# Optimization experiments

Measured on AMD Instinct MI355X. Metric: run time of the kernel, lower is better.

## Reference

```python
import jax, jax.numpy as jnp
import numpy as np

B, T, E = 256, 33, 1024
L = T - 1  # one distinct LSTM per timestep


def setup_inputs() -> dict:
    key = jax.random.key(0)
    k1, k2, k3, k4 = jax.random.split(key, 4)
    scale = 1.0 / np.sqrt(E)  # matches nn.LSTM default uniform init
    return {
        "input_feature_vectors": jax.random.normal(k1, (B, T, E), jnp.float32),
        "target_feature_vector": jax.random.normal(k2, (B, E), jnp.float32),
        "W_ih": jax.random.uniform(k3, (L, 4 * E, E), jnp.float32, -scale, scale),
        "W_hh": jax.random.uniform(k4, (L, 4 * E, E), jnp.float32, -scale, scale),
    }


def _lstm_step(carry, inp):
    h, c = carry                      # [B, E] each
    x_t, w_ih, w_hh = inp             # [B, E], [4E, E], [4E, E]
    gates = x_t @ w_ih.T + h @ w_hh.T  # [B, 4E]; bias=False in the original
    i, f, g, o = jnp.split(gates, 4, axis=-1)  # torch gate order: i, f, g, o
    i = jax.nn.sigmoid(i)
    f = jax.nn.sigmoid(f)
    g = jnp.tanh(g)
    o = jax.nn.sigmoid(o)
    c = f * c + i * g
    h = o * jnp.tanh(c)
    return (h, c), None


def reference(input_feature_vectors, target_feature_vector, W_ih, W_hh):
    x = input_feature_vectors
    b, t, e = x.shape
    h0 = jnp.zeros((b, e), x.dtype)            # h_0 = zeros(1, B, E)
    c0 = x[:, 1, :]                            # c_0 = input[:, 1:2, :].transpose(0,1)
    xs = jnp.swapaxes(x[:, : t - 1, :], 0, 1)  # [T-1, B, E], steps 0..T-2
    (h, c), _ = jax.lax.scan(_lstm_step, (h0, c0), (xs, W_ih, W_hh))
    # output[:, 0, :] of the last step is the final h
    loss = jnp.mean(jnp.abs(h - target_feature_vector))  # L1Loss (mean)
    return loss, h, c
```

## Files before the change

kernel.cpp:

```cpp
#include <hip/hip_runtime.h>
#include <hip/hip_bf16.h>

typedef __attribute__((ext_vector_type(8))) short bf16x8;
typedef __attribute__((ext_vector_type(4))) float f32x4;
typedef __attribute__((ext_vector_type(16))) float f32x16;

static constexpr int BB = 256;
static constexpr int TT = 33;
static constexpr int EE = 1024;
static constexpr int LL = 32;
static constexpr int NG = 4096;

static constexpr int BUF_SZ   = 24576;
static constexpr int A_OFF    = 16384;
static constexpr int RED_OFF  = 98304;
static constexpr int LDSG_OFF = 131072;
static constexpr int HH_OFF   = 147456;
static constexpr int LDS_DYN  = 149504;

__device__ __forceinline__ short f2bf(float f) {
  unsigned u = __builtin_bit_cast(unsigned, f);
  u += 0x7fffu + ((u >> 16) & 1u);
  return (short)(u >> 16);
}

__device__ __forceinline__ bf16x8 cvt8(f32x4 a, f32x4 b) {
  bf16x8 r;
  r[0] = f2bf(a[0]); r[1] = f2bf(a[1]); r[2] = f2bf(a[2]); r[3] = f2bf(a[3]);
  r[4] = f2bf(b[0]); r[5] = f2bf(b[1]); r[6] = f2bf(b[2]); r[7] = f2bf(b[3]);
  return r;
}

__device__ __forceinline__ float sigm(float x) { return 1.0f / (1.0f + __expf(-x)); }
__device__ __forceinline__ float tanh_f(float x) { return 1.0f - 2.0f / (__expf(2.0f * x) + 1.0f); }

__global__ __launch_bounds__(256) void lstm_prep(
    const float* __restrict__ x, short* __restrict__ xbf, float* __restrict__ c_io,
    unsigned* __restrict__ flags)
{
  if (blockIdx.x == 0) flags[(size_t)threadIdx.x * 64] = 0;
  int gth = blockIdx.x * 256 + threadIdx.x;
  int eb  = gth & 127;
  int row = (gth >> 7) & 255;
  int t   = gth >> 15;
  const float* src = x + ((size_t)row * TT + t) * EE + (eb << 3);
  f32x4 lo = *(const f32x4*)src;
  f32x4 hi = *(const f32x4*)(src + 4);
  *(bf16x8*)(xbf + ((size_t)t * BB + row) * EE + (eb << 3)) = cvt8(lo, hi);
  if (t == 1) {
    float* cd = c_io + (size_t)row * EE + (eb << 3);
    *(f32x4*)cd = lo;
    *(f32x4*)(cd + 4) = hi;
  }
}

__global__ __launch_bounds__(512) void lstm_rec(
    const short* __restrict__ xbf,
    const float* __restrict__ Wih,
    const float* __restrict__ Whh,
    short* __restrict__ hroll,
    float* __restrict__ c_io,
    float* __restrict__ h_out,
    unsigned* __restrict__ flags)
{
  extern __shared__ __align__(16) char smem[];

  const int tid  = threadIdx.x;
  const int lane = tid & 63;
  const int wv   = tid >> 6;
  const int ct   = wv & 1;
  const int kh   = wv >> 1;

  const int wg     = blockIdx.x;
  const int xcd    = wg & 7;
  const int jj     = wg >> 3;
  const int rowgrp = jj & 3;
  const int ehi    = jj >> 2;
  const int e0     = (xcd * 8 + ehi) << 4;
  const int row0   = rowgrp << 6;

  size_t wsrc_off[2]; int wdst_off[2];
#pragma unroll
  for (int r = 0; r < 2; ++r) {
    int o = r * 8192 + wv * 1024 + lane * 16;
    int lrow = o >> 8;
    int mwr = ((lrow & 7) << 5) | ((lrow & 8) << 1);
    wsrc_off[r] = (size_t)((lrow >> 4) * EE + e0 + (lrow & 15)) * 4096 + ((o & 255) ^ mwr);
    wdst_off[r] = r * 8192 + wv * 1024;
  }
  size_t asrc_off; int adst_off;
  {
    int o = wv * 1024 + lane * 16;
    int lrow = o >> 7;
    asrc_off = (size_t)(row0 + lrow) * 2048 + ((o & 127) ^ ((lrow & 7) << 4));
    adst_off = A_OFF + wv * 1024;
  }

  const int wrow    = ct * 32 + (lane & 31);
  const int mwr2    = ((wrow & 7) << 5) | ((wrow & 8) << 1);
  const int kW      = kh * 64 + ((lane >> 5) << 5);
  const int woff_lo = wrow * 256 + (kW ^ mwr2);
  const int woff_hi = wrow * 256 + ((kW + 16) ^ mwr2);
  const int arow    = lane & 31;
  const int kA      = kh * 32 + ((lane >> 5) << 4);
  const int aoff0   = arow * 128 + (kA ^ ((arow & 7) << 4));
  const int aoff1   = aoff0 + 4096;

  const int er  = tid & 63;
  const int ee_ = tid >> 6;
  float c0r = c_io[(size_t)(row0 + er) * EE + e0 + ee_];
  float c1r = c_io[(size_t)(row0 + er) * EE + e0 + ee_ + 8];

  f32x16 acc0{}, acc1{};

  auto stageC = [&](int tt, int cc, int buf) {
    const int p  = cc >> 4;
    const int k0 = (cc & 15) << 6;
    const char* Wt = (const char*)((p ? Whh : Wih) + (size_t)tt * NG * EE);
    const char* At = p ? (const char*)(hroll + (size_t)(tt - 1) * BB * EE)
                       : (const char*)(xbf + (size_t)tt * BB * EE);
    char* dst = smem + buf * BUF_SZ;
#pragma unroll
    for (int r = 0; r < 2; ++r)
      __builtin_amdgcn_global_load_lds(
          (const __attribute__((address_space(1))) unsigned int*)(Wt + wsrc_off[r] + (k0 << 2)),
          (__attribute__((address_space(3))) unsigned int*)(dst + wdst_off[r]), 16, 0, 0);
    __builtin_amdgcn_global_load_lds(
        (const __attribute__((address_space(1))) unsigned int*)(At + asrc_off + (k0 << 1)),
        (__attribute__((address_space(3))) unsigned int*)(dst + adst_off), 16, 0, 0);
  };

  auto compute = [&](int buf) {
    const char* Wb = smem + buf * BUF_SZ;
    const char* Ab = Wb + A_OFF;
    f32x4 wlo = *(const f32x4*)(Wb + woff_lo);
    f32x4 whi = *(const f32x4*)(Wb + woff_hi);
    bf16x8 bfr = cvt8(wlo, whi);
    bf16x8 a0 = *(const bf16x8*)(Ab + aoff0);
    bf16x8 a1 = *(const bf16x8*)(Ab + aoff1);
    acc0 = __builtin_amdgcn_mfma_f32_32x32x16_bf16(a0, bfr, acc0, 0, 0, 0);
    acc1 = __builtin_amdgcn_mfma_f32_32x32x16_bf16(a1, bfr, acc1, 0, 0, 0);
  };

  float* red = (float*)(smem + RED_OFF);
  const int rsw = (lane & 3) << 4;
  auto slotp = [&](int src, int rt) { return red + (size_t)(((ct * 2 + src) * 2 + rt)) * 1024; };
  auto dumpT = [&](float* base, const f32x16& a) {
    char* b = (char*)base + lane * 64;
#pragma unroll
    for (int jq = 0; jq < 4; ++jq) {
      f32x4 v{a[jq * 4 + 0], a[jq * 4 + 1], a[jq * 4 + 2], a[jq * 4 + 3]};
      *(f32x4*)(b + ((jq * 16) ^ rsw)) = v;
    }
  };
  auto addT = [&](const float* base, f32x16& a) {
    const char* b = (const char*)base + lane * 64;
#pragma unroll
    for (int jq = 0; jq < 4; ++jq) {
      f32x4 v = *(const f32x4*)(b + ((jq * 16) ^ rsw));
      a[jq * 4 + 0] += v[0]; a[jq * 4 + 1] += v[1];
      a[jq * 4 + 2] += v[2]; a[jq * 4 + 3] += v[3];
    }
  };

  stageC(0, 0, 0);
  stageC(0, 1, 1);
  stageC(0, 2, 2);

  int fc = 0;
  for (int t = 0; t < LL; ++t) {
    const int nch = t ? 32 : 16;
    for (int c = 0; c < nch; ++c, ++fc) {
      if (t == LL - 1 && c == nch - 1)      asm volatile("s_waitcnt vmcnt(0)" ::: "memory");
      else if (t == LL - 1 && c == nch - 2) asm volatile("s_waitcnt vmcnt(3)" ::: "memory");
      else                                   asm volatile("s_waitcnt vmcnt(6)" ::: "memory");
      __builtin_amdgcn_s_barrier();
      compute(fc & 3);

      int sc = c + 3, st = t;
      if (sc >= nch) { sc -= nch; st = t + 1; }
      bool skip = (st > t && sc == 2) || (st >= LL);
      if (!skip) {
        if (st == t && sc == 16) {
          if (tid < 256) {
            while (__hip_atomic_load(flags + (size_t)tid * 64,
                                     __ATOMIC_RELAXED, __HIP_MEMORY_SCOPE_AGENT) < (unsigned)t)
              __builtin_amdgcn_s_sleep(1);
          }
          __builtin_amdgcn_s_barrier();
          __builtin_amdgcn_sched_barrier(0);
        }
        stageC(st, sc, (fc + 3) & 3);
      }
    }

    if (kh >= 2) { dumpT(slotp(kh - 2, 0), acc0); dumpT(slotp(kh - 2, 1), acc1); }
    asm volatile("s_waitcnt lgkmcnt(0)" ::: "memory");
    __builtin_amdgcn_s_barrier();
    if (kh < 2) { addT(slotp(kh, 0), acc0); addT(slotp(kh, 1), acc1); }
    asm volatile("s_waitcnt lgkmcnt(0)" ::: "memory");
    __builtin_amdgcn_s_barrier();
    if (kh == 1) { dumpT(slotp(0, 0), acc0); dumpT(slotp(0, 1), acc1); }
    asm volatile("s_waitcnt lgkmcnt(0)" ::: "memory");
    __builtin_amdgcn_s_barrier();
    if (kh == 0) {
      addT(slotp(0, 0), acc0);
      addT(slotp(0, 1), acc1);
      const int swc = mwr2;
      char* gb = (char*)(smem + LDSG_OFF) + wrow * 256;
#pragma unroll
      for (int rt = 0; rt < 2; ++rt) {
        const f32x16& a = rt ? acc1 : acc0;
#pragma unroll
        for (int jq = 0; jq < 4; ++jq) {
          int rowb = rt * 128 + jq * 32 + ((lane >> 5) << 4);
          f32x4 v{a[jq * 4 + 0], a[jq * 4 + 1], a[jq * 4 + 2], a[jq * 4 + 3]};
          *(f32x4*)(gb + (rowb ^ swc)) = v;
        }
      }
    }
    acc0 = f32x16{}; acc1 = f32x16{};
    asm volatile("s_waitcnt lgkmcnt(0)" ::: "memory");
    __builtin_amdgcn_s_barrier();

    {
      const char* gbase = (const char*)(smem + LDSG_OFF);
      short* hh = (short*)(smem + HH_OFF);
      auto gate = [&](int g, int ee) {
        int wc = g * 16 + ee;
        int swc = ((wc & 7) << 5) | ((wc & 8) << 1);
        return *(const float*)(gbase + wc * 256 + ((er * 4) ^ swc));
      };
      float gi0 = gate(0, ee_), gf0 = gate(1, ee_), gg0 = gate(2, ee_), go0 = gate(3, ee_);
      float gi1 = gate(0, ee_ + 8), gf1 = gate(1, ee_ + 8), gg1 = gate(2, ee_ + 8), go1 = gate(3, ee_ + 8);

      c0r = sigm(gf0) * c0r + sigm(gi0) * tanh_f(gg0);
      float h0n = sigm(go0) * tanh_f(c0r);
      c1r = sigm(gf1) * c1r + sigm(gi1) * tanh_f(gg1);
      float h1n = sigm(go1) * tanh_f(c1r);

      hh[er * 16 + ee_]     = f2bf(h0n);
      hh[er * 16 + ee_ + 8] = f2bf(h1n);

      if (t == LL - 1) {
        size_t o0 = (size_t)(row0 + er) * EE + e0 + ee_;
        size_t o1 = o0 + 8;
        h_out[o0] = h0n; c_io[o0] = c0r;
        h_out[o1] = h1n; c_io[o1] = c1r;
      }
    }
    asm volatile("s_waitcnt lgkmcnt(0)" ::: "memory");
    __builtin_amdgcn_s_barrier();

    if (t < LL - 1) {
      if (tid < 256) {
        int r = tid >> 2, q = tid & 3;
        unsigned long long v = *(const unsigned long long*)(smem + HH_OFF + r * 32 + q * 8);
        __hip_atomic_store(
            (unsigned long long*)((char*)hroll + ((size_t)t * BB + row0 + r) * 2048 + (size_t)e0 * 2 + q * 8),
            v, __ATOMIC_RELAXED, __HIP_MEMORY_SCOPE_AGENT);
      }
      stageC(t + 1, 2, (fc + 2) & 3);
      asm volatile("s_waitcnt vmcnt(3)" ::: "memory");
      __builtin_amdgcn_s_barrier();
      if (tid == 0)
        __hip_atomic_store(flags + (size_t)wg * 64, (unsigned)(t + 1),
                           __ATOMIC_RELAXED, __HIP_MEMORY_SCOPE_AGENT);
    }
  }
}

__global__ __launch_bounds__(256) void lstm_loss_part(
    const float* __restrict__ h, const float* __restrict__ tgt, float* __restrict__ partials)
{
  __shared__ float lds[4];
  int tid = threadIdx.x;
  float s = 0.f;
  int base = blockIdx.x * 1024 + tid;
#pragma unroll
  for (int q = 0; q < 4; ++q) {
    int idx = base + (q << 8);
    s += fabsf(h[idx] - tgt[idx]);
  }
#pragma unroll
  for (int off = 32; off > 0; off >>= 1) s += __shfl_down(s, off, 64);
  if ((tid & 63) == 0) lds[tid >> 6] = s;
  __syncthreads();
  if (tid == 0) partials[blockIdx.x] = lds[0] + lds[1] + lds[2] + lds[3];
}

__global__ __launch_bounds__(256) void lstm_loss_fin(
    const float* __restrict__ partials, float* __restrict__ out)
{
  __shared__ float lds[4];
  int tid = threadIdx.x;
  float s = partials[tid];
#pragma unroll
  for (int off = 32; off > 0; off >>= 1) s += __shfl_down(s, off, 64);
  if ((tid & 63) == 0) lds[tid >> 6] = s;
  __syncthreads();
  if (tid == 0) out[0] = (lds[0] + lds[1] + lds[2] + lds[3]) * (1.0f / 262144.0f);
}

extern "C" void kernel_launch(void* const* d_in, const int* in_sizes, int n_in,
                              void* d_out, int out_size, void* d_ws, size_t ws_size,
                              hipStream_t stream) {
  const float* x   = (const float*)d_in[0];
  const float* tgt = (const float*)d_in[1];
  const float* Wih = (const float*)d_in[2];
  const float* Whh = (const float*)d_in[3];

  float* out   = (float*)d_out;
  float* h_out = out + 1;
  float* c_io  = out + 1 + BB * EE;

  short* xbf      = (short*)d_ws;
  short* hroll    = (short*)((char*)xbf + (size_t)LL * BB * EE * 2);
  float* partials = (float*)((char*)hroll + (size_t)LL * BB * EE * 2);
  unsigned* flags = (unsigned*)((char*)partials + 1024);

  static bool attr_done = false;
  if (!attr_done) {
    hipFuncSetAttribute((const void*)lstm_rec,
                        hipFuncAttributeMaxDynamicSharedMemorySize, LDS_DYN);
    attr_done = true;
  }

  lstm_prep<<<4096, 256, 0, stream>>>(x, xbf, c_io, flags);

  {
    const short* xbfA = xbf; const float* WihA = Wih; const float* WhhA = Whh;
    short* hrollA = hroll; float* cA = c_io; float* hA = h_out; unsigned* flagsA = flags;
    void* args[] = {&xbfA, &WihA, &WhhA, &hrollA, &cA, &hA, &flagsA};
    hipError_t e = hipLaunchCooperativeKernel((void*)lstm_rec, dim3(256), dim3(512),
                                              args, LDS_DYN, stream);
    if (e != hipSuccess)
      lstm_rec<<<256, 512, LDS_DYN, stream>>>(xbf, Wih, Whh, hroll, c_io, h_out, flags);
  }

  lstm_loss_part<<<256, 256, 0, stream>>>(h_out, tgt, partials);
  lstm_loss_fin<<<1, 256, 0, stream>>>(partials, out);
}
```

Before: 609.4 us.

## Process K-chunks in pairs with six LDS buffers and reuse buffers for reduction

Each barrier now covers two K-chunks, with a six-deep LDS ring buffer replacing the four-deep one, so the main loop needs half as many barriers and waitcnt stalls. The cross-wave reduction scratch and the gate/h staging area now live in free ring buffers instead of dedicated LDS regions, which shrinks total LDS. The A-tile layout and swizzle are remapped so two rows share a 256-byte line, which changes the bank-conflict pattern. The cost is deeper in-flight prefetch, more complex buffer indexing, and a risk of buffer aliasing races at step boundaries.

```diff
diff --git a/kernel.cpp b/kernel.cpp
--- a/kernel.cpp
+++ b/kernel.cpp
@@ -11,12 +11,10 @@
 static constexpr int LL = 32;
 static constexpr int NG = 4096;
 
-static constexpr int BUF_SZ   = 24576;
-static constexpr int A_OFF    = 16384;
-static constexpr int RED_OFF  = 98304;
-static constexpr int LDSG_OFF = 131072;
-static constexpr int HH_OFF   = 147456;
-static constexpr int LDS_DYN  = 149504;
+static constexpr int BUF_SZ  = 24576;
+static constexpr int A_OFF   = 16384;
+static constexpr int NBUF    = 6;
+static constexpr int LDS_DYN = 147456;
 
 __device__ __forceinline__ short f2bf(float f) {
   unsigned u = __builtin_bit_cast(unsigned, f);
@@ -90,10 +88,14 @@
   }
   size_t asrc_off; int adst_off;
   {
-    int o = wv * 1024 + lane * 16;
-    int lrow = o >> 7;
-    asrc_off = (size_t)(row0 + lrow) * 2048 + ((o & 127) ^ ((lrow & 7) << 4));
-    adst_off = A_OFF + wv * 1024;
+    int o  = wv * 1024 + lane * 16;
+    int G  = o >> 4;
+    int rp = G >> 4;
+    int s  = G & 15;
+    int r  = rp * 2 + (s & 1);
+    int g  = ((s >> 1) ^ (rp & 7)) & 7;
+    asrc_off = (size_t)(row0 + r) * 2048 + g * 16;
+    adst_off = A_OFF + o;
   }
 
   const int wrow    = ct * 32 + (lane & 31);
@@ -102,9 +104,10 @@
   const int woff_lo = wrow * 256 + (kW ^ mwr2);
   const int woff_hi = wrow * 256 + ((kW + 16) ^ mwr2);
   const int arow    = lane & 31;
-  const int kA      = kh * 32 + ((lane >> 5) << 4);
-  const int aoff0   = arow * 128 + (kA ^ ((arow & 7) << 4));
-  const int aoff1   = aoff0 + 4096;
+  const int rpA     = arow >> 1;
+  const int gkh     = kh * 2 + (lane >> 5);
+  const int sA      = (2 * gkh + (arow & 1)) ^ ((rpA & 7) << 1);
+  const int aoff0   = rpA * 256 + sA * 16;
 
   const int er  = tid & 63;
   const int ee_ = tid >> 6;
@@ -137,14 +140,12 @@
     f32x4 whi = *(const f32x4*)(Wb + woff_hi);
     bf16x8 bfr = cvt8(wlo, whi);
     bf16x8 a0 = *(const bf16x8*)(Ab + aoff0);
-    bf16x8 a1 = *(const bf16x8*)(Ab + aoff1);
+    bf16x8 a1 = *(const bf16x8*)(Ab + aoff0 + 4096);
     acc0 = __builtin_amdgcn_mfma_f32_32x32x16_bf16(a0, bfr, acc0, 0, 0, 0);
     acc1 = __builtin_amdgcn_mfma_f32_32x32x16_bf16(a1, bfr, acc1, 0, 0, 0);
   };
 
-  float* red = (float*)(smem + RED_OFF);
-  const int rsw = (lane & 3) << 4;
-  auto slotp = [&](int src, int rt) { return red + (size_t)(((ct * 2 + src) * 2 + rt)) * 1024; };
+  const int rsw = ((lane >> 1) & 3) << 4;
   auto dumpT = [&](float* base, const f32x16& a) {
     char* b = (char*)base + lane * 64;
 #pragma unroll
@@ -163,25 +164,23 @@
     }
   };
 
-  stageC(0, 0, 0);
-  stageC(0, 1, 1);
-  stageC(0, 2, 2);
-
-  int fc = 0;
+  stageC(0, 0, 0); stageC(0, 1, 1); stageC(0, 2, 2); stageC(0, 3, 3);
+
+  int fb = 0;
   for (int t = 0; t < LL; ++t) {
     const int nch = t ? 32 : 16;
-    for (int c = 0; c < nch; ++c, ++fc) {
-      if (t == LL - 1 && c == nch - 1)      asm volatile("s_waitcnt vmcnt(0)" ::: "memory");
-      else if (t == LL - 1 && c == nch - 2) asm volatile("s_waitcnt vmcnt(3)" ::: "memory");
+    for (int pc = 0; pc < nch / 2; ++pc) {
+      if (t == LL - 1 && pc == nch / 2 - 1) asm volatile("s_waitcnt vmcnt(0)" ::: "memory");
       else                                   asm volatile("s_waitcnt vmcnt(6)" ::: "memory");
       __builtin_amdgcn_s_barrier();
-      compute(fc & 3);
-
-      int sc = c + 3, st = t;
-      if (sc >= nch) { sc -= nch; st = t + 1; }
-      bool skip = (st > t && sc == 2) || (st >= LL);
+      compute(fb);
+      compute((fb + 1) % NBUF);
+
+      int sc0 = 2 * pc + 4, st = t;
+      if (sc0 >= nch) { sc0 -= nch; st = t + 1; }
+      bool skip = (st > t && sc0 == 2) || (st >= LL);
       if (!skip) {
-        if (st == t && sc == 16) {
+        if (st == t && sc0 == 16) {
           if (tid < 256) {
             while (__hip_atomic_load(flags + (size_t)tid * 64,
                                      __ATOMIC_RELAXED, __HIP_MEMORY_SCOPE_AGENT) < (unsigned)t)
@@ -190,9 +189,15 @@
           __builtin_amdgcn_s_barrier();
           __builtin_amdgcn_sched_barrier(0);
         }
-        stageC(st, sc, (fc + 3) & 3);
+        stageC(st, sc0,     (fb + 4) % NBUF);
+        stageC(st, sc0 + 1, (fb + 5) % NBUF);
       }
-    }
+      fb = (fb + 2) % NBUF;
+    }
+
+    float* red  = (float*)(smem + (size_t)((fb + 4) % NBUF) * BUF_SZ);
+    char*  glsb = smem + (size_t)((fb + 5) % NBUF) * BUF_SZ;
+    auto slotp = [&](int src, int rt) { return red + (size_t)((ct * 2 + src) * 2 + rt) * 1024; };
 
     if (kh >= 2) { dumpT(slotp(kh - 2, 0), acc0); dumpT(slotp(kh - 2, 1), acc1); }
     asm volatile("s_waitcnt lgkmcnt(0)" ::: "memory");
@@ -206,8 +211,7 @@
     if (kh == 0) {
       addT(slotp(0, 0), acc0);
       addT(slotp(0, 1), acc1);
-      const int swc = mwr2;
-      char* gb = (char*)(smem + LDSG_OFF) + wrow * 256;
+      char* gb = glsb + wrow * 256;
 #pragma unroll
       for (int rt = 0; rt < 2; ++rt) {
         const f32x16& a = rt ? acc1 : acc0;
@@ -215,7 +219,7 @@
         for (int jq = 0; jq < 4; ++jq) {
           int rowb = rt * 128 + jq * 32 + ((lane >> 5) << 4);
           f32x4 v{a[jq * 4 + 0], a[jq * 4 + 1], a[jq * 4 + 2], a[jq * 4 + 3]};
-          *(f32x4*)(gb + (rowb ^ swc)) = v;
+          *(f32x4*)(gb + (rowb ^ mwr2)) = v;
         }
       }
     }
@@ -224,12 +228,11 @@
     __builtin_amdgcn_s_barrier();
 
     {
-      const char* gbase = (const char*)(smem + LDSG_OFF);
-      short* hh = (short*)(smem + HH_OFF);
+      short* hh = (short*)(glsb + 16384);
       auto gate = [&](int g, int ee) {
         int wc = g * 16 + ee;
         int swc = ((wc & 7) << 5) | ((wc & 8) << 1);
-        return *(const float*)(gbase + wc * 256 + ((er * 4) ^ swc));
+        return *(const float*)(glsb + wc * 256 + ((er * 4) ^ swc));
       };
       float gi0 = gate(0, ee_), gf0 = gate(1, ee_), gg0 = gate(2, ee_), go0 = gate(3, ee_);
       float gi1 = gate(0, ee_ + 8), gf1 = gate(1, ee_ + 8), gg1 = gate(2, ee_ + 8), go1 = gate(3, ee_ + 8);
@@ -255,13 +258,14 @@
     if (t < LL - 1) {
       if (tid < 256) {
         int r = tid >> 2, q = tid & 3;
-        unsigned long long v = *(const unsigned long long*)(smem + HH_OFF + r * 32 + q * 8);
+        unsigned long long v = *(const unsigned long long*)(glsb + 16384 + r * 32 + q * 8);
         __hip_atomic_store(
             (unsigned long long*)((char*)hroll + ((size_t)t * BB + row0 + r) * 2048 + (size_t)e0 * 2 + q * 8),
             v, __ATOMIC_RELAXED, __HIP_MEMORY_SCOPE_AGENT);
       }
-      stageC(t + 1, 2, (fc + 2) & 3);
-      asm volatile("s_waitcnt vmcnt(3)" ::: "memory");
+      stageC(t + 1, 2, (fb + 2) % NBUF);
+      stageC(t + 1, 3, (fb + 3) % NBUF);
+      asm volatile("s_waitcnt vmcnt(6)" ::: "memory");
       __builtin_amdgcn_s_barrier();
       if (tid == 0)
         __hip_atomic_store(flags + (size_t)wg * 64, (unsigned)(t + 1),
```

Result: faster. 542.8 us (median of 2 runs) (-10.9%).
